# Kernel optimization log

Measured on AMD Instinct MI355X. Metric: run time of the kernel, lower is better.

## Reference

```python
import jax, jax.numpy as jnp
import numpy as np

SLOPE = 0.01  # nn.LeakyReLU(negative_slope=0.01)
B, D, H, E, NH = 16384, 17, 256, 64, 4  # batch, input_dim, hidden, embed, heads

def lrelu(x):
    return jnp.where(x >= 0, x, SLOPE * x)

def setup_inputs() -> dict:
    key = jax.random.key(0)
    ks = jax.random.split(key, 16)
    s = 0.08  # ~xavier-ish scale for these widths
    return {
        "x":   jax.random.normal(ks[0], (B, D), jnp.float32),
        # per-dimension subnets, batched over the D=17 subnet axis
        "W1":  jax.random.normal(ks[1], (D, H), jnp.float32) * 1.0,      # 1 -> H
        "b1":  jnp.zeros((D, H), jnp.float32),
        "Wm":  jax.random.normal(ks[2], (2, D, H, H), jnp.float32) * s,  # two middle H->H layers
        "bm":  jnp.zeros((2, D, H), jnp.float32),
        "Wf":  jax.random.normal(ks[3], (D, H, E), jnp.float32) * s,     # H -> output_dim(=E)
        "bf":  jnp.zeros((D, E), jnp.float32),
        # MultiheadAttention in/out projections (torch Linear convention: y = x @ W.T + b)
        "Wq":  jax.random.normal(ks[4], (E, E), jnp.float32) * s,
        "bq":  jnp.zeros((E,), jnp.float32),
        "Wk":  jax.random.normal(ks[5], (E, E), jnp.float32) * s,
        "bk":  jnp.zeros((E,), jnp.float32),
        "Wv":  jax.random.normal(ks[6], (E, E), jnp.float32) * s,
        "bv":  jnp.zeros((E,), jnp.float32),
        "Wo":  jax.random.normal(ks[7], (E, E), jnp.float32) * s,
        "bo":  jnp.zeros((E,), jnp.float32),
        "Wfc": jax.random.normal(ks[8], (E, 1), jnp.float32) * s,
        "bfc": jnp.zeros((1,), jnp.float32),
    }

def reference(x, W1, b1, Wm, bm, Wf, bf, Wq, bq, Wk, bk, Wv, bv, Wo, bo, Wfc, bfc):
    b, d = x.shape
    # batched tiny subnets: first layer is (B,D,1) x (D,1,H) == outer product
    h = lrelu(x[:, :, None] * W1[None] + b1)                    # (B,D,H)
    for l in range(Wm.shape[0]):                                 # fixed 2 middle layers
        h = lrelu(jnp.einsum('bih,iho->bio', h, Wm[l]) + bm[l])  # (B,D,H)
    tokens = jnp.einsum('bih,iho->bio', h, Wf) + bf              # (B,D,E); proj is None (dims match)
    # self-attention (torch MultiheadAttention, batch_first)
    hd = E // NH
    def heads(t):
        return t.reshape(b, d, NH, hd).transpose(0, 2, 1, 3)     # (B,NH,D,hd)
    q = heads(tokens @ Wq.T + bq)
    k = heads(tokens @ Wk.T + bk)
    v = heads(tokens @ Wv.T + bv)
    scores = jnp.einsum('bhqd,bhkd->bhqk', q, k) / jnp.sqrt(jnp.asarray(hd, x.dtype))
    attn = jax.nn.softmax(scores, axis=-1)                       # (B,NH,D,D)
    o = jnp.einsum('bhqk,bhkd->bhqd', attn, v)
    o = o.transpose(0, 2, 1, 3).reshape(b, d, E) @ Wo.T + bo     # (B,D,E)
    pooled = o.mean(axis=1)                                      # (B,E)
    return lrelu(pooled @ Wfc + bfc)                             # (B,1)
```

## Files before the change

### kernel.cpp

```cpp
#include <hip/hip_runtime.h>
#include <hip/hip_bf16.h>

#define B_N   16384
#define D_N   17
#define H_N   256
#define E_N   64

typedef __attribute__((ext_vector_type(8))) short bf16x8;
typedef __attribute__((ext_vector_type(4))) float f32x4;

#define WAITV(N) asm volatile("s_waitcnt vmcnt(" #N ")" ::: "memory")
#define WAITL()  asm volatile("s_waitcnt lgkmcnt(0)" ::: "memory")
#define BAR()    __builtin_amdgcn_s_barrier()

static __device__ __forceinline__ short f2bf(float f){
  unsigned u = __builtin_bit_cast(unsigned, f);
  unsigned r = (u + 0x7fffu + ((u >> 16) & 1u)) >> 16;
  return (short)(unsigned short)r;
}
static __device__ __forceinline__ float bf2f(short s){
  unsigned u = ((unsigned)(unsigned short)s) << 16;
  return __builtin_bit_cast(float, u);
}
static __device__ __forceinline__ float lrelu(float v){ return fmaxf(v, 0.01f * v); }

static __device__ __forceinline__ void gload_lds16(const short* g, short* l){
  __builtin_amdgcn_global_load_lds(
      (const __attribute__((address_space(1))) unsigned int*)g,
      (__attribute__((address_space(3))) unsigned int*)l, 16, 0, 0);
}

__global__ void transpose_convert(const float* __restrict__ in, short* __restrict__ outp,
                                  int R, int C){
  __shared__ float tile[32][33];
  int g = blockIdx.z;
  const float* inp = in + (size_t)g * R * C;
  short* op = outp + (size_t)g * R * C;
  int c0 = blockIdx.x * 32, r0 = blockIdx.y * 32;
  for (int i = threadIdx.y; i < 32; i += 8)
    tile[i][threadIdx.x] = inp[(size_t)(r0 + i) * C + c0 + threadIdx.x];
  __syncthreads();
  for (int i = threadIdx.y; i < 32; i += 8)
    op[(size_t)(c0 + i) * R + r0 + threadIdx.x] = f2bf(tile[threadIdx.x][i]);
}

__global__ void convert_wqkv(const float* __restrict__ Wq, const float* __restrict__ Wk,
                             const float* __restrict__ Wv, short* __restrict__ outw){
  int i = blockIdx.x * 256 + threadIdx.x;
  int g = i >> 12, r = i & 4095;
  const float* W = (g == 0) ? Wq : (g == 1 ? Wk : Wv);
  outw[i] = f2bf(W[r]);
}

__global__ void wcomb_kernel(const float* __restrict__ Wo, const float* __restrict__ Wfc,
                             const float* __restrict__ bo, const float* __restrict__ bfc,
                             float* __restrict__ wcomb){
  int e = threadIdx.x;
  float acc = 0.f;
  for (int eo = 0; eo < 64; ++eo) acc += Wo[eo * 64 + e] * Wfc[eo];
  wcomb[e] = acc;
  if (e == 0){
    float bc = bfc[0];
    for (int eo = 0; eo < 64; ++eo) bc += bo[eo] * Wfc[eo];
    wcomb[64] = bc;
  }
}

static __device__ __forceinline__ void stage_w256(const short* Wt, int kk, short* wb,
                                                  int tid, int wave){
  #pragma unroll
  for (int r = 0; r < 4; ++r){
    int li = r * 256 + tid;
    int n  = li >> 2;
    int cc = (li & 3) ^ ((n >> 1) & 3);
    gload_lds16(Wt + n * 256 + kk * 32 + cc * 8,
                wb + (size_t)(r * 256 + wave * 64) * 8);
  }
}
static __device__ __forceinline__ void stage_w64(const short* Wt, int kk, short* wb,
                                                 int tid, int wave){
  int n  = tid >> 2;
  int cc = (tid & 3) ^ ((n >> 1) & 3);
  gload_lds16(Wt + n * 256 + kk * 32 + cc * 8, wb + (size_t)(wave * 64) * 8);
}

__global__ __launch_bounds__(256, 2) void subnet_kernel(
    const float* __restrict__ x, const float* __restrict__ W1, const float* __restrict__ b1,
    const float* __restrict__ bm, const float* __restrict__ bf_,
    const float* __restrict__ bq, const float* __restrict__ bk, const float* __restrict__ bv,
    const short* __restrict__ WmT, const short* __restrict__ WfT, const short* __restrict__ Wqkv,
    short* __restrict__ qkv)
{
  __shared__ short hbuf[64 * 256];
  __shared__ short wbuf[3][256 * 32];

  int wg = blockIdx.x;
  int idx = (wg & 7) * 544 + (wg >> 3);
  const int d  = idx >> 8;
  const int m0 = (idx & 255) * 64;

  const int tid = threadIdx.x;
  const int lane = tid & 63, wave = tid >> 6;
  const int l15 = lane & 15, lhi = lane >> 4;

  const short* WtL0 = WmT + (size_t)(0 * D_N + d) * (H_N * H_N);
  const short* WtL1 = WmT + (size_t)(1 * D_N + d) * (H_N * H_N);
  const short* Wfd  = WfT + (size_t)d * (E_N * H_N);

  stage_w256(WtL0, 0, &wbuf[0][0], tid, wave);
  stage_w256(WtL0, 1, &wbuf[1][0], tid, wave);

  {
    const int kp = tid & 127;
    const int mh = tid >> 7;
    const float w1a = W1[d * H_N + 2 * kp], w1b = W1[d * H_N + 2 * kp + 1];
    const float b1a = b1[d * H_N + 2 * kp], b1b = b1[d * H_N + 2 * kp + 1];
    #pragma unroll
    for (int i = 0; i < 32; ++i){
      int m = mh * 32 + i;
      float xv = x[(size_t)(m0 + m) * D_N + d];
      unsigned lo = (unsigned short)f2bf(lrelu(xv * w1a + b1a));
      unsigned hi = (unsigned short)f2bf(lrelu(xv * w1b + b1b));
      int byte = m * 512 + ((((kp >> 2) ^ (m & 7))) << 4) + ((kp & 3) << 2);
      *(unsigned*)((char*)&hbuf[0] + byte) = lo | (hi << 16);
    }
  }
  WAITL();

  for (int L = 0; L < 2; ++L){
    const float* bias = bm + (size_t)(L * D_N + d) * H_N;
    f32x4 acc[4][4];
    #pragma unroll
    for (int a = 0; a < 4; ++a)
      #pragma unroll
      for (int c = 0; c < 4; ++c) acc[a][c] = (f32x4){0.f, 0.f, 0.f, 0.f};

    for (int kk = 0; kk < 8; ++kk){
      const int s = L * 8 + kk;
      if (L == 1 && kk == 7) { WAITV(1); } else { WAITV(4); }
      BAR();
      const int s2 = s + 2;
      if (s2 < 8)       stage_w256(WtL0, s2,     &wbuf[s2 % 3][0], tid, wave);
      else if (s2 < 16) stage_w256(WtL1, s2 - 8, &wbuf[s2 % 3][0], tid, wave);
      else              stage_w64 (Wfd,  s2 - 16,&wbuf[s2 % 3][0], tid, wave);

      const short* wb = &wbuf[s % 3][0];
      bf16x8 af[4], bfr[4];
      #pragma unroll
      for (int fr = 0; fr < 4; ++fr){
        int row = fr * 16 + l15;
        int cch = kk * 4 + lhi;
        af[fr] = *(const bf16x8*)((const char*)&hbuf[0] + row * 512 + ((cch ^ (row & 7)) << 4));
      }
      #pragma unroll
      for (int fc = 0; fc < 4; ++fc){
        int n = wave * 64 + fc * 16 + l15;
        bfr[fc] = *(const bf16x8*)((const char*)wb + n * 64 + ((lhi ^ ((n >> 1) & 3)) << 4));
      }
      #pragma unroll
      for (int fr = 0; fr < 4; ++fr)
        #pragma unroll
        for (int fc = 0; fc < 4; ++fc)
          acc[fr][fc] = __builtin_amdgcn_mfma_f32_16x16x32_bf16(af[fr], bfr[fc], acc[fr][fc], 0, 0, 0);
    }
    BAR();
    #pragma unroll
    for (int fr = 0; fr < 4; ++fr)
      #pragma unroll
      for (int fc = 0; fc < 4; ++fc)
        #pragma unroll
        for (int j = 0; j < 4; ++j){
          int row = fr * 16 + lhi * 4 + j;
          int col = wave * 64 + fc * 16 + l15;
          float v = lrelu(acc[fr][fc][j] + bias[col]);
          int byte = row * 512 + ((((col >> 3) ^ (row & 7))) << 4) + ((col & 7) << 1);
          *(short*)((char*)&hbuf[0] + byte) = f2bf(v);
        }
    WAITL();
  }

  {
    const int r0 = wave * 16;
    f32x4 acc[4];
    #pragma unroll
    for (int fc = 0; fc < 4; ++fc) acc[fc] = (f32x4){0.f, 0.f, 0.f, 0.f};
    for (int kk = 0; kk < 8; ++kk){
      if (kk == 7) { WAITV(0); } else { WAITV(1); }
      BAR();
      if (kk < 6) stage_w64(Wfd, kk + 2, &wbuf[(18 + kk) % 3][0], tid, wave);
      const short* wb = &wbuf[(16 + kk) % 3][0];
      int row = r0 + l15;
      int cch = kk * 4 + lhi;
      bf16x8 a = *(const bf16x8*)((const char*)&hbuf[0] + row * 512 + ((cch ^ (row & 7)) << 4));
      #pragma unroll
      for (int fc = 0; fc < 4; ++fc){
        int n = fc * 16 + l15;
        bf16x8 b = *(const bf16x8*)((const char*)wb + n * 64 + ((lhi ^ ((n >> 1) & 3)) << 4));
        acc[fc] = __builtin_amdgcn_mfma_f32_16x16x32_bf16(a, b, acc[fc], 0, 0, 0);
      }
    }
    BAR();
    #pragma unroll
    for (int fc = 0; fc < 4; ++fc)
      #pragma unroll
      for (int j = 0; j < 4; ++j){
        int row = r0 + lhi * 4 + j;
        int col = fc * 16 + l15;
        float v = acc[fc][j] + bf_[d * E_N + col];
        int byte = row * 128 + ((((col >> 3) ^ (row & 7))) << 4) + ((col & 7) << 1);
        *(short*)((char*)&hbuf[0] + byte) = f2bf(v);
      }
    WAITL();
    BAR();
  }

  {
    f32x4 acc[4][3];
    #pragma unroll
    for (int fr = 0; fr < 4; ++fr)
      #pragma unroll
      for (int fc = 0; fc < 3; ++fc) acc[fr][fc] = (f32x4){0.f, 0.f, 0.f, 0.f};
    #pragma unroll
    for (int kk = 0; kk < 2; ++kk){
      bf16x8 af[4];
      #pragma unroll
      for (int fr = 0; fr < 4; ++fr){
        int row = fr * 16 + l15;
        int cch = kk * 4 + lhi;
        af[fr] = *(const bf16x8*)((const char*)&hbuf[0] + row * 128 + ((cch ^ (row & 7)) << 4));
      }
      bf16x8 bb[3];
      #pragma unroll
      for (int fc = 0; fc < 3; ++fc){
        int n = wave * 48 + fc * 16 + l15;
        bb[fc] = *(const bf16x8*)(Wqkv + (size_t)n * E_N + kk * 32 + lhi * 8);
      }
      #pragma unroll
      for (int fr = 0; fr < 4; ++fr)
        #pragma unroll
        for (int fc = 0; fc < 3; ++fc)
          acc[fr][fc] = __builtin_amdgcn_mfma_f32_16x16x32_bf16(af[fr], bb[fc], acc[fr][fc], 0, 0, 0);
    }
    #pragma unroll
    for (int fr = 0; fr < 4; ++fr)
      #pragma unroll
      for (int fc = 0; fc < 3; ++fc)
        #pragma unroll
        for (int j = 0; j < 4; ++j){
          int n = wave * 48 + fc * 16 + l15;
          int g = n >> 6, nl = n & 63;
          float bias = (g == 0) ? bq[nl] : (g == 1 ? bk[nl] : bv[nl]);
          int bg = m0 + fr * 16 + lhi * 4 + j;
          float v = acc[fr][fc][j] + bias;
          qkv[((size_t)bg * D_N + d) * 192 + n] = f2bf(v);
        }
  }
}

__global__ __launch_bounds__(256, 2) void attn_kernel(
    const short* __restrict__ qkv, const float* __restrict__ wc, float* __restrict__ out)
{
  __shared__ short smem[4][17 * 192];
  const int tid = threadIdx.x, lane = tid & 63, wave = tid >> 6;
  const int h = lane >> 4, iq = lane & 15;

  const int b = blockIdx.x * 4 + wave;
  const short* src = qkv + (size_t)b * (17 * 192);
  for (int g0 = lane; g0 < 408; g0 += 64){
    int i = g0 / 24, c = g0 % 24;
    bf16x8 v = *(const bf16x8*)(src + g0 * 8);
    *(bf16x8*)((char*)&smem[wave][0] + i * 384 + ((c ^ (i & 7)) << 4)) = v;
  }

  float vt = 0.f, vt16 = 0.f;
  #pragma unroll
  for (int u2 = 0; u2 < 2; ++u2){
    int cch = 16 + 2 * h + u2;
    bf16x8 vj  = *(const bf16x8*)((char*)&smem[wave][0] + iq * 384 + ((cch ^ (iq & 7)) << 4));
    bf16x8 v16 = *(const bf16x8*)((char*)&smem[wave][0] + 16 * 384 + (cch << 4));
    #pragma unroll
    for (int z = 0; z < 8; ++z){
      float w = wc[h * 16 + u2 * 8 + z];
      vt   += bf2f(vj[z])  * w;
      vt16 += bf2f(v16[z]) * w;
    }
  }

  float part = 0.f;
  #pragma unroll 1
  for (int t = 0; t < 2; ++t){
    const int i = (t == 0) ? iq : 16;
    float q[16];
    #pragma unroll
    for (int u2 = 0; u2 < 2; ++u2){
      int cch = 2 * h + u2;
      bf16x8 v = *(const bf16x8*)((char*)&smem[wave][0] + i * 384 + ((cch ^ (i & 7)) << 4));
      #pragma unroll
      for (int z = 0; z < 8; ++z) q[u2 * 8 + z] = bf2f(v[z]);
    }
    float num = 0.f, den = 0.f;
    #pragma unroll 1
    for (int j = 0; j < 16; ++j){
      float a2 = 0.f;
      #pragma unroll
      for (int u2 = 0; u2 < 2; ++u2){
        int cch = 8 + 2 * h + u2;
        bf16x8 v = *(const bf16x8*)((char*)&smem[wave][0] + j * 384 + ((cch ^ (j & 7)) << 4));
        #pragma unroll
        for (int z = 0; z < 8; ++z) a2 += q[u2 * 8 + z] * bf2f(v[z]);
      }
      float e = __expf(a2 * 0.25f);
      num += e * __shfl(vt, (lane & 48) + j);
      den += e;
    }
    {
      float a2 = 0.f;
      #pragma unroll
      for (int u2 = 0; u2 < 2; ++u2){
        int cch = 8 + 2 * h + u2;
        bf16x8 v = *(const bf16x8*)((char*)&smem[wave][0] + 16 * 384 + (cch << 4));
        #pragma unroll
        for (int z = 0; z < 8; ++z) a2 += q[u2 * 8 + z] * bf2f(v[z]);
      }
      float e = __expf(a2 * 0.25f);
      num += e * vt16;
      den += e;
    }
    float contrib = num / den;
    part += (t == 0 || iq == 0) ? contrib : 0.f;
  }
  #pragma unroll
  for (int off = 1; off < 64; off <<= 1) part += __shfl_xor(part, off);
  if (lane == 0) out[b] = lrelu(part * (1.f / 17.f) + wc[64]);
}

extern "C" void kernel_launch(void* const* d_in, const int* in_sizes, int n_in,
                              void* d_out, int out_size, void* d_ws, size_t ws_size,
                              hipStream_t stream)
{
  const float* x   = (const float*)d_in[0];
  const float* W1  = (const float*)d_in[1];
  const float* b1  = (const float*)d_in[2];
  const float* Wm  = (const float*)d_in[3];
  const float* bm  = (const float*)d_in[4];
  const float* Wf  = (const float*)d_in[5];
  const float* bf_ = (const float*)d_in[6];
  const float* Wq  = (const float*)d_in[7];
  const float* bq  = (const float*)d_in[8];
  const float* Wk  = (const float*)d_in[9];
  const float* bk  = (const float*)d_in[10];
  const float* Wv  = (const float*)d_in[11];
  const float* bv  = (const float*)d_in[12];
  const float* Wo  = (const float*)d_in[13];
  const float* bo  = (const float*)d_in[14];
  const float* Wfc = (const float*)d_in[15];
  const float* bfc = (const float*)d_in[16];
  float* out = (float*)d_out;
  (void)in_sizes; (void)n_in; (void)out_size; (void)ws_size;

  char* ws = (char*)d_ws;
  size_t off = 0;
  auto alloc = [&](size_t bytes) -> char* {
    char* p = ws + off;
    off = (off + bytes + 255) & ~(size_t)255;
    return p;
  };
  short* qkvb  = (short*)alloc((size_t)B_N * D_N * 192 * 2);
  short* WmT   = (short*)alloc((size_t)2 * D_N * H_N * H_N * 2);
  short* WfT   = (short*)alloc((size_t)D_N * E_N * H_N * 2);
  short* Wqkvb = (short*)alloc((size_t)192 * E_N * 2);
  float* wcomb = (float*)alloc(65 * sizeof(float));

  transpose_convert<<<dim3(8, 8, 2 * D_N), dim3(32, 8), 0, stream>>>(Wm, WmT, 256, 256);
  transpose_convert<<<dim3(2, 8, D_N),     dim3(32, 8), 0, stream>>>(Wf, WfT, 256, 64);
  convert_wqkv<<<dim3(48), dim3(256), 0, stream>>>(Wq, Wk, Wv, Wqkvb);
  wcomb_kernel<<<dim3(1), dim3(64), 0, stream>>>(Wo, Wfc, bo, bfc, wcomb);

  subnet_kernel<<<dim3(256 * D_N), dim3(256), 0, stream>>>(
      x, W1, b1, bm, bf_, bq, bk, bv, WmT, WfT, Wqkvb, qkvb);

  attn_kernel<<<dim3(4096), dim3(256), 0, stream>>>(qkvb, wcomb, out);
}
```

Measured before the change: 233.6 us.

## Double subnet row tile to 128 per block, sharing staged weights across two halves

The subnet kernel now runs 512 threads per block on 128 batch rows. Two groups of four waves each own a 64-row activation buffer and read the same LDS-staged weight tiles. This halves the global-to-LDS weight traffic per row and the number of blocks, and the Wf staging is regrouped into pairs of k-slices so each load step uses all 512 threads. The cost is doubled LDS for activations and larger blocks, which may lower occupancy, and barriers now span eight waves.

Result: slower. 244.1 us (+4.5%).

```diff
diff --git a/kernel.cpp b/kernel.cpp
--- a/kernel.cpp
+++ b/kernel.cpp
@@ -69,39 +69,44 @@
 static __device__ __forceinline__ void stage_w256(const short* Wt, int kk, short* wb,
                                                   int tid, int wave){
   #pragma unroll
-  for (int r = 0; r < 4; ++r){
-    int li = r * 256 + tid;
+  for (int r = 0; r < 2; ++r){
+    int li = r * 512 + tid;
     int n  = li >> 2;
     int cc = (li & 3) ^ ((n >> 1) & 3);
     gload_lds16(Wt + n * 256 + kk * 32 + cc * 8,
-                wb + (size_t)(r * 256 + wave * 64) * 8);
-  }
-}
-static __device__ __forceinline__ void stage_w64(const short* Wt, int kk, short* wb,
-                                                 int tid, int wave){
-  int n  = tid >> 2;
-  int cc = (tid & 3) ^ ((n >> 1) & 3);
-  gload_lds16(Wt + n * 256 + kk * 32 + cc * 8, wb + (size_t)(wave * 64) * 8);
-}
-
-__global__ __launch_bounds__(256, 2) void subnet_kernel(
+                wb + (size_t)(r * 512 + wave * 64) * 8);
+  }
+}
+static __device__ __forceinline__ void stage_wf_pair(const short* Wfd, int kk0, short* wb,
+                                                     int tid, int wave){
+  int sub = tid >> 8;
+  int u   = tid & 255;
+  int n   = u >> 2;
+  int cc  = (u & 3) ^ ((n >> 1) & 3);
+  gload_lds16(Wfd + n * 256 + (kk0 + sub) * 32 + cc * 8,
+              wb + sub * 2048 + (size_t)((wave & 3) * 64) * 8);
+}
+
+__global__ __launch_bounds__(512, 2) void subnet_kernel(
     const float* __restrict__ x, const float* __restrict__ W1, const float* __restrict__ b1,
     const float* __restrict__ bm, const float* __restrict__ bf_,
     const float* __restrict__ bq, const float* __restrict__ bk, const float* __restrict__ bv,
     const short* __restrict__ WmT, const short* __restrict__ WfT, const short* __restrict__ Wqkv,
     short* __restrict__ qkv)
 {
-  __shared__ short hbuf[64 * 256];
+  __shared__ short hbuf[2][64 * 256];
   __shared__ short wbuf[3][256 * 32];
 
   int wg = blockIdx.x;
-  int idx = (wg & 7) * 544 + (wg >> 3);
-  const int d  = idx >> 8;
-  const int m0 = (idx & 255) * 64;
+  int idx = (wg & 7) * 272 + (wg >> 3);
+  const int d  = idx >> 7;
+  const int m0 = (idx & 127) * 128;
 
   const int tid = threadIdx.x;
   const int lane = tid & 63, wave = tid >> 6;
+  const int mh = wave >> 2, wv = wave & 3;
   const int l15 = lane & 15, lhi = lane >> 4;
+  short* hb = &hbuf[mh][0];
 
   const short* WtL0 = WmT + (size_t)(0 * D_N + d) * (H_N * H_N);
   const short* WtL1 = WmT + (size_t)(1 * D_N + d) * (H_N * H_N);
@@ -112,17 +117,19 @@
 
   {
     const int kp = tid & 127;
-    const int mh = tid >> 7;
+    const int mq = tid >> 7;
+    const int tl = mq >> 1, half = mq & 1;
+    short* hp = &hbuf[tl][0];
     const float w1a = W1[d * H_N + 2 * kp], w1b = W1[d * H_N + 2 * kp + 1];
     const float b1a = b1[d * H_N + 2 * kp], b1b = b1[d * H_N + 2 * kp + 1];
     #pragma unroll
     for (int i = 0; i < 32; ++i){
-      int m = mh * 32 + i;
-      float xv = x[(size_t)(m0 + m) * D_N + d];
+      int m = half * 32 + i;
+      float xv = x[(size_t)(m0 + tl * 64 + m) * D_N + d];
       unsigned lo = (unsigned short)f2bf(lrelu(xv * w1a + b1a));
       unsigned hi = (unsigned short)f2bf(lrelu(xv * w1b + b1b));
       int byte = m * 512 + ((((kp >> 2) ^ (m & 7))) << 4) + ((kp & 3) << 2);
-      *(unsigned*)((char*)&hbuf[0] + byte) = lo | (hi << 16);
+      *(unsigned*)((char*)hp + byte) = lo | (hi << 16);
     }
   }
   WAITL();
@@ -137,12 +144,12 @@
 
     for (int kk = 0; kk < 8; ++kk){
       const int s = L * 8 + kk;
-      if (L == 1 && kk == 7) { WAITV(1); } else { WAITV(4); }
+      if (s == 15) { WAITV(1); } else { WAITV(2); }
       BAR();
       const int s2 = s + 2;
-      if (s2 < 8)       stage_w256(WtL0, s2,     &wbuf[s2 % 3][0], tid, wave);
-      else if (s2 < 16) stage_w256(WtL1, s2 - 8, &wbuf[s2 % 3][0], tid, wave);
-      else              stage_w64 (Wfd,  s2 - 16,&wbuf[s2 % 3][0], tid, wave);
+      if (s2 < 8)       stage_w256(WtL0, s2,            &wbuf[s2 % 3][0], tid, wave);
+      else if (s2 < 16) stage_w256(WtL1, s2 - 8,        &wbuf[s2 % 3][0], tid, wave);
+      else              stage_wf_pair(Wfd, (s2 - 16) * 2, &wbuf[s2 % 3][0], tid, wave);
 
       const short* wb = &wbuf[s % 3][0];
       bf16x8 af[4], bfr[4];
@@ -150,11 +157,11 @@
       for (int fr = 0; fr < 4; ++fr){
         int row = fr * 16 + l15;
         int cch = kk * 4 + lhi;
-        af[fr] = *(const bf16x8*)((const char*)&hbuf[0] + row * 512 + ((cch ^ (row & 7)) << 4));
+        af[fr] = *(const bf16x8*)((const char*)hb + row * 512 + ((cch ^ (row & 7)) << 4));
       }
       #pragma unroll
       for (int fc = 0; fc < 4; ++fc){
-        int n = wave * 64 + fc * 16 + l15;
+        int n = wv * 64 + fc * 16 + l15;
         bfr[fc] = *(const bf16x8*)((const char*)wb + n * 64 + ((lhi ^ ((n >> 1) & 3)) << 4));
       }
       #pragma unroll
@@ -171,32 +178,37 @@
         #pragma unroll
         for (int j = 0; j < 4; ++j){
           int row = fr * 16 + lhi * 4 + j;
-          int col = wave * 64 + fc * 16 + l15;
+          int col = wv * 64 + fc * 16 + l15;
           float v = lrelu(acc[fr][fc][j] + bias[col]);
           int byte = row * 512 + ((((col >> 3) ^ (row & 7))) << 4) + ((col & 7) << 1);
-          *(short*)((char*)&hbuf[0] + byte) = f2bf(v);
+          *(short*)((char*)hb + byte) = f2bf(v);
         }
     WAITL();
   }
 
   {
-    const int r0 = wave * 16;
+    const int r0 = wv * 16;
     f32x4 acc[4];
     #pragma unroll
     for (int fc = 0; fc < 4; ++fc) acc[fc] = (f32x4){0.f, 0.f, 0.f, 0.f};
-    for (int kk = 0; kk < 8; ++kk){
-      if (kk == 7) { WAITV(0); } else { WAITV(1); }
+    for (int t = 0; t < 4; ++t){
+      if (t == 3) { WAITV(0); } else { WAITV(1); }
       BAR();
-      if (kk < 6) stage_w64(Wfd, kk + 2, &wbuf[(18 + kk) % 3][0], tid, wave);
-      const short* wb = &wbuf[(16 + kk) % 3][0];
-      int row = r0 + l15;
-      int cch = kk * 4 + lhi;
-      bf16x8 a = *(const bf16x8*)((const char*)&hbuf[0] + row * 512 + ((cch ^ (row & 7)) << 4));
-      #pragma unroll
-      for (int fc = 0; fc < 4; ++fc){
-        int n = fc * 16 + l15;
-        bf16x8 b = *(const bf16x8*)((const char*)wb + n * 64 + ((lhi ^ ((n >> 1) & 3)) << 4));
-        acc[fc] = __builtin_amdgcn_mfma_f32_16x16x32_bf16(a, b, acc[fc], 0, 0, 0);
+      if (t < 2) stage_wf_pair(Wfd, (t + 2) * 2, &wbuf[(18 + t) % 3][0], tid, wave);
+      const short* wbase = &wbuf[(16 + t) % 3][0];
+      #pragma unroll
+      for (int kkh = 0; kkh < 2; ++kkh){
+        int kk = 2 * t + kkh;
+        int row = r0 + l15;
+        int cch = kk * 4 + lhi;
+        bf16x8 a = *(const bf16x8*)((const char*)hb + row * 512 + ((cch ^ (row & 7)) << 4));
+        const short* wbs = wbase + kkh * 2048;
+        #pragma unroll
+        for (int fc = 0; fc < 4; ++fc){
+          int n = fc * 16 + l15;
+          bf16x8 b = *(const bf16x8*)((const char*)wbs + n * 64 + ((lhi ^ ((n >> 1) & 3)) << 4));
+          acc[fc] = __builtin_amdgcn_mfma_f32_16x16x32_bf16(a, b, acc[fc], 0, 0, 0);
+        }
       }
     }
     BAR();
@@ -208,7 +220,7 @@
         int col = fc * 16 + l15;
         float v = acc[fc][j] + bf_[d * E_N + col];
         int byte = row * 128 + ((((col >> 3) ^ (row & 7))) << 4) + ((col & 7) << 1);
-        *(short*)((char*)&hbuf[0] + byte) = f2bf(v);
+        *(short*)((char*)hb + byte) = f2bf(v);
       }
     WAITL();
     BAR();
@@ -227,12 +239,12 @@
       for (int fr = 0; fr < 4; ++fr){
         int row = fr * 16 + l15;
         int cch = kk * 4 + lhi;
-        af[fr] = *(const bf16x8*)((const char*)&hbuf[0] + row * 128 + ((cch ^ (row & 7)) << 4));
+        af[fr] = *(const bf16x8*)((const char*)hb + row * 128 + ((cch ^ (row & 7)) << 4));
       }
       bf16x8 bb[3];
       #pragma unroll
       for (int fc = 0; fc < 3; ++fc){
-        int n = wave * 48 + fc * 16 + l15;
+        int n = wv * 48 + fc * 16 + l15;
         bb[fc] = *(const bf16x8*)(Wqkv + (size_t)n * E_N + kk * 32 + lhi * 8);
       }
       #pragma unroll
@@ -247,10 +259,10 @@
       for (int fc = 0; fc < 3; ++fc)
         #pragma unroll
         for (int j = 0; j < 4; ++j){
-          int n = wave * 48 + fc * 16 + l15;
+          int n = wv * 48 + fc * 16 + l15;
           int g = n >> 6, nl = n & 63;
           float bias = (g == 0) ? bq[nl] : (g == 1 ? bk[nl] : bv[nl]);
-          int bg = m0 + fr * 16 + lhi * 4 + j;
+          int bg = m0 + mh * 64 + fr * 16 + lhi * 4 + j;
           float v = acc[fr][fc][j] + bias;
           qkv[((size_t)bg * D_N + d) * 192 + n] = f2bf(v);
         }
@@ -376,7 +388,7 @@
   convert_wqkv<<<dim3(48), dim3(256), 0, stream>>>(Wq, Wk, Wv, Wqkvb);
   wcomb_kernel<<<dim3(1), dim3(64), 0, stream>>>(Wo, Wfc, bo, bfc, wcomb);
 
-  subnet_kernel<<<dim3(256 * D_N), dim3(256), 0, stream>>>(
+  subnet_kernel<<<dim3(128 * D_N), dim3(512), 0, stream>>>(
       x, W1, b1, bm, bf_, bq, bk, bv, WmT, WfT, Wqkvb, qkvb);
 
   attn_kernel<<<dim3(4096), dim3(256), 0, stream>>>(qkvb, wcomb, out);
```

## Load subnet weight fragments directly into registers instead of staging through LDS

Applied to the files above, without the earlier changes.

Removes the triple-buffered LDS weight staging (global_load_lds plus per-step barriers) and instead has each wave load its B-operand fragments straight from global memory into registers, double-buffered two k-steps ahead. Freeing 48KB of LDS lets occupancy rise to 3 blocks per CU via launch bounds. The cost is uncoalesced 16-byte global reads per lane, more VGPR pressure from the register double buffer, and reliance on L1/L2 for weight reuse across waves.

Measured after the change: 449.6 us. 92.4% more time.

```diff
diff --git a/kernel.cpp b/kernel.cpp
--- a/kernel.cpp
+++ b/kernel.cpp
@@ -9,7 +9,6 @@
 typedef __attribute__((ext_vector_type(8))) short bf16x8;
 typedef __attribute__((ext_vector_type(4))) float f32x4;
 
-#define WAITV(N) asm volatile("s_waitcnt vmcnt(" #N ")" ::: "memory")
 #define WAITL()  asm volatile("s_waitcnt lgkmcnt(0)" ::: "memory")
 #define BAR()    __builtin_amdgcn_s_barrier()
 
@@ -23,12 +22,6 @@
   return __builtin_bit_cast(float, u);
 }
 static __device__ __forceinline__ float lrelu(float v){ return fmaxf(v, 0.01f * v); }
-
-static __device__ __forceinline__ void gload_lds16(const short* g, short* l){
-  __builtin_amdgcn_global_load_lds(
-      (const __attribute__((address_space(1))) unsigned int*)g,
-      (__attribute__((address_space(3))) unsigned int*)l, 16, 0, 0);
-}
 
 __global__ void transpose_convert(const float* __restrict__ in, short* __restrict__ outp,
                                   int R, int C){
@@ -66,33 +59,21 @@
   }
 }
 
-static __device__ __forceinline__ void stage_w256(const short* Wt, int kk, short* wb,
-                                                  int tid, int wave){
+static __device__ __forceinline__ void ldB(bf16x8* b, const short* base,
+                                           const int* off, int kk){
   #pragma unroll
-  for (int r = 0; r < 4; ++r){
-    int li = r * 256 + tid;
-    int n  = li >> 2;
-    int cc = (li & 3) ^ ((n >> 1) & 3);
-    gload_lds16(Wt + n * 256 + kk * 32 + cc * 8,
-                wb + (size_t)(r * 256 + wave * 64) * 8);
-  }
-}
-static __device__ __forceinline__ void stage_w64(const short* Wt, int kk, short* wb,
-                                                 int tid, int wave){
-  int n  = tid >> 2;
-  int cc = (tid & 3) ^ ((n >> 1) & 3);
-  gload_lds16(Wt + n * 256 + kk * 32 + cc * 8, wb + (size_t)(wave * 64) * 8);
-}
-
-__global__ __launch_bounds__(256, 2) void subnet_kernel(
-    const float* __restrict__ x, const float* __restrict__ W1, const float* __restrict__ b1,
+  for (int fc = 0; fc < 4; ++fc)
+    b[fc] = *(const bf16x8*)(base + off[fc] + kk * 32);
+}
+
+__global__ __launch_bounds__(256, 3) void subnet_kernel(
+    const float* __restrict__ x, const float* __restrict__ W1, const float* __restrict__ b1v,
     const float* __restrict__ bm, const float* __restrict__ bf_,
     const float* __restrict__ bq, const float* __restrict__ bk, const float* __restrict__ bv,
     const short* __restrict__ WmT, const short* __restrict__ WfT, const short* __restrict__ Wqkv,
     short* __restrict__ qkv)
 {
   __shared__ short hbuf[64 * 256];
-  __shared__ short wbuf[3][256 * 32];
 
   int wg = blockIdx.x;
   int idx = (wg & 7) * 544 + (wg >> 3);
@@ -107,27 +88,37 @@
   const short* WtL1 = WmT + (size_t)(1 * D_N + d) * (H_N * H_N);
   const short* Wfd  = WfT + (size_t)d * (E_N * H_N);
 
-  stage_w256(WtL0, 0, &wbuf[0][0], tid, wave);
-  stage_w256(WtL0, 1, &wbuf[1][0], tid, wave);
+  int off[4], offW[4];
+  #pragma unroll
+  for (int fc = 0; fc < 4; ++fc){
+    off[fc]  = (wave * 64 + fc * 16 + l15) * 256 + lhi * 8;
+    offW[fc] = (fc * 16 + l15) * 256 + lhi * 8;
+  }
+
+  bf16x8 bb0[4], bb1[4];
+  ldB(bb0, WtL0, off, 0);
+  ldB(bb1, WtL0, off, 1);
 
   {
     const int kp = tid & 127;
     const int mh = tid >> 7;
-    const float w1a = W1[d * H_N + 2 * kp], w1b = W1[d * H_N + 2 * kp + 1];
-    const float b1a = b1[d * H_N + 2 * kp], b1b = b1[d * H_N + 2 * kp + 1];
+    const float w1a = W1[d * H_N + 2 * kp],  w1b = W1[d * H_N + 2 * kp + 1];
+    const float c1a = b1v[d * H_N + 2 * kp], c1b = b1v[d * H_N + 2 * kp + 1];
     #pragma unroll
     for (int i = 0; i < 32; ++i){
       int m = mh * 32 + i;
       float xv = x[(size_t)(m0 + m) * D_N + d];
-      unsigned lo = (unsigned short)f2bf(lrelu(xv * w1a + b1a));
-      unsigned hi = (unsigned short)f2bf(lrelu(xv * w1b + b1b));
+      unsigned lo = (unsigned short)f2bf(lrelu(xv * w1a + c1a));
+      unsigned hi = (unsigned short)f2bf(lrelu(xv * w1b + c1b));
       int byte = m * 512 + ((((kp >> 2) ^ (m & 7))) << 4) + ((kp & 3) << 2);
       *(unsigned*)((char*)&hbuf[0] + byte) = lo | (hi << 16);
     }
   }
   WAITL();
+  BAR();
 
   for (int L = 0; L < 2; ++L){
+    const short* Wt = L ? WtL1 : WtL0;
     const float* bias = bm + (size_t)(L * D_N + d) * H_N;
     f32x4 acc[4][4];
     #pragma unroll
@@ -135,33 +126,21 @@
       #pragma unroll
       for (int c = 0; c < 4; ++c) acc[a][c] = (f32x4){0.f, 0.f, 0.f, 0.f};
 
+    #pragma unroll
     for (int kk = 0; kk < 8; ++kk){
-      const int s = L * 8 + kk;
-      if (L == 1 && kk == 7) { WAITV(1); } else { WAITV(4); }
-      BAR();
-      const int s2 = s + 2;
-      if (s2 < 8)       stage_w256(WtL0, s2,     &wbuf[s2 % 3][0], tid, wave);
-      else if (s2 < 16) stage_w256(WtL1, s2 - 8, &wbuf[s2 % 3][0], tid, wave);
-      else              stage_w64 (Wfd,  s2 - 16,&wbuf[s2 % 3][0], tid, wave);
-
-      const short* wb = &wbuf[s % 3][0];
-      bf16x8 af[4], bfr[4];
+      bf16x8* bc = (kk & 1) ? bb1 : bb0;
       #pragma unroll
       for (int fr = 0; fr < 4; ++fr){
         int row = fr * 16 + l15;
         int cch = kk * 4 + lhi;
-        af[fr] = *(const bf16x8*)((const char*)&hbuf[0] + row * 512 + ((cch ^ (row & 7)) << 4));
-      }
-      #pragma unroll
-      for (int fc = 0; fc < 4; ++fc){
-        int n = wave * 64 + fc * 16 + l15;
-        bfr[fc] = *(const bf16x8*)((const char*)wb + n * 64 + ((lhi ^ ((n >> 1) & 3)) << 4));
-      }
-      #pragma unroll
-      for (int fr = 0; fr < 4; ++fr)
+        bf16x8 a = *(const bf16x8*)((const char*)&hbuf[0] + row * 512 + ((cch ^ (row & 7)) << 4));
         #pragma unroll
         for (int fc = 0; fc < 4; ++fc)
-          acc[fr][fc] = __builtin_amdgcn_mfma_f32_16x16x32_bf16(af[fr], bfr[fc], acc[fr][fc], 0, 0, 0);
+          acc[fr][fc] = __builtin_amdgcn_mfma_f32_16x16x32_bf16(a, bc[fc], acc[fr][fc], 0, 0, 0);
+      }
+      if (kk < 6)       ldB(bc, Wt, off, kk + 2);
+      else if (L == 0)  ldB(bc, WtL1, off, kk - 6);
+      else              ldB(bc, Wfd, offW, kk - 6);
     }
     BAR();
     #pragma unroll
@@ -177,6 +156,7 @@
           *(short*)((char*)&hbuf[0] + byte) = f2bf(v);
         }
     WAITL();
+    BAR();
   }
 
   {
@@ -184,20 +164,16 @@
     f32x4 acc[4];
     #pragma unroll
     for (int fc = 0; fc < 4; ++fc) acc[fc] = (f32x4){0.f, 0.f, 0.f, 0.f};
+    #pragma unroll
     for (int kk = 0; kk < 8; ++kk){
-      if (kk == 7) { WAITV(0); } else { WAITV(1); }
-      BAR();
-      if (kk < 6) stage_w64(Wfd, kk + 2, &wbuf[(18 + kk) % 3][0], tid, wave);
-      const short* wb = &wbuf[(16 + kk) % 3][0];
+      bf16x8* bc = (kk & 1) ? bb1 : bb0;
       int row = r0 + l15;
       int cch = kk * 4 + lhi;
       bf16x8 a = *(const bf16x8*)((const char*)&hbuf[0] + row * 512 + ((cch ^ (row & 7)) << 4));
       #pragma unroll
-      for (int fc = 0; fc < 4; ++fc){
-        int n = fc * 16 + l15;
-        bf16x8 b = *(const bf16x8*)((const char*)wb + n * 64 + ((lhi ^ ((n >> 1) & 3)) << 4));
-        acc[fc] = __builtin_amdgcn_mfma_f32_16x16x32_bf16(a, b, acc[fc], 0, 0, 0);
-      }
+      for (int fc = 0; fc < 4; ++fc)
+        acc[fc] = __builtin_amdgcn_mfma_f32_16x16x32_bf16(a, bc[fc], acc[fc], 0, 0, 0);
+      if (kk < 6) ldB(bc, Wfd, offW, kk + 2);
     }
     BAR();
     #pragma unroll
@@ -229,17 +205,17 @@
         int cch = kk * 4 + lhi;
         af[fr] = *(const bf16x8*)((const char*)&hbuf[0] + row * 128 + ((cch ^ (row & 7)) << 4));
       }
-      bf16x8 bb[3];
+      bf16x8 bqkv[3];
       #pragma unroll
       for (int fc = 0; fc < 3; ++fc){
         int n = wave * 48 + fc * 16 + l15;
-        bb[fc] = *(const bf16x8*)(Wqkv + (size_t)n * E_N + kk * 32 + lhi * 8);
+        bqkv[fc] = *(const bf16x8*)(Wqkv + (size_t)n * E_N + kk * 32 + lhi * 8);
       }
       #pragma unroll
       for (int fr = 0; fr < 4; ++fr)
         #pragma unroll
         for (int fc = 0; fc < 3; ++fc)
-          acc[fr][fc] = __builtin_amdgcn_mfma_f32_16x16x32_bf16(af[fr], bb[fc], acc[fr][fc], 0, 0, 0);
+          acc[fr][fc] = __builtin_amdgcn_mfma_f32_16x16x32_bf16(af[fr], bqkv[fc], acc[fr][fc], 0, 0, 0);
     }
     #pragma unroll
     for (int fr = 0; fr < 4; ++fr)
```
